# Performance work log

Measured on AMD Instinct MI355X. Metric: run time of the kernel, lower is better.

The kernel has to match this reference:

```python
import jax, jax.numpy as jnp
import numpy as np

IN_FEATURES = 1024
OUT_FEATURES = 1024
NUM_GRIDS = 8
GRID_MIN, GRID_MAX = -2.0, 2.0
DENOM = (GRID_MAX - GRID_MIN) / (NUM_GRIDS - 1)
LN_EPS = 1e-5
GRID = jnp.linspace(GRID_MIN, GRID_MAX, NUM_GRIDS)


def setup_inputs() -> dict:
    key = jax.random.key(0)
    k_x, k_sw, k_bw = jax.random.split(key, 3)
    N = 8192
    x = jax.random.normal(k_x, (N, IN_FEATURES), dtype=jnp.float32)
    ln_gamma = jnp.ones((IN_FEATURES,), dtype=jnp.float32)
    ln_beta = jnp.zeros((IN_FEATURES,), dtype=jnp.float32)
    # trunc_normal(std=0.1) approximated by scaled normal
    spline_w = 0.1 * jax.random.normal(k_sw, (OUT_FEATURES, IN_FEATURES * NUM_GRIDS), dtype=jnp.float32)
    base_w = jax.random.normal(k_bw, (OUT_FEATURES, IN_FEATURES), dtype=jnp.float32) * (1.0 / np.sqrt(IN_FEATURES))
    base_b = jnp.zeros((OUT_FEATURES,), dtype=jnp.float32)
    return {"x": x, "ln_gamma": ln_gamma, "ln_beta": ln_beta,
            "spline_w": spline_w, "base_w": base_w, "base_b": base_b}


def reference(x, ln_gamma, ln_beta, spline_w, base_w, base_b):
    # LayerNorm over last dim
    mu = jnp.mean(x, axis=-1, keepdims=True)
    var = jnp.var(x, axis=-1, keepdims=True)
    xn = (x - mu) * jax.lax.rsqrt(var + LN_EPS) * ln_gamma + ln_beta
    # RBF basis: [N, in, G]
    basis = jnp.exp(-jnp.square((xn[..., None] - GRID) / DENOM))
    basis = basis.reshape(x.shape[0], IN_FEATURES * NUM_GRIDS)
    y = jnp.einsum('nk,ok->no', basis, spline_w)
    y = y + jnp.einsum('nd,od->no', jax.nn.silu(x), base_w) + base_b
    return y
```

## Files before the change

kernel.cpp:

```cpp
#include <hip/hip_runtime.h>
#include <hip/hip_bf16.h>
#include <stdint.h>

#define IN_F 1024
#define OUT_F 1024
#define NG 8
#define KSPLINE 8192
#define KDIM 9216
#define KHALF 4608
#define M_ROWS 8192
#define LOG2E 1.4426950408889634f
#define KC 2.1019642153762872f

#define A_BLOCKS (M_ROWS / 4)
#define W_BLOCKS ((OUT_F * 2304) / 256)
#define RB (KDIM * 2)

using half4v = __attribute__((ext_vector_type(4))) _Float16;
using half8  = __attribute__((ext_vector_type(8))) _Float16;
using f32x4  = __attribute__((ext_vector_type(4))) float;

#define AS1 __attribute__((address_space(1)))
#define AS3 __attribute__((address_space(3)))

__global__ __launch_bounds__(256) void prep_kernel(
        const float* __restrict__ x, const float* __restrict__ gamma,
        const float* __restrict__ beta, const float* __restrict__ sw,
        const float* __restrict__ bw, _Float16* __restrict__ A,
        _Float16* __restrict__ W) {
    if (blockIdx.x >= A_BLOCKS) {
        int idx = (blockIdx.x - A_BLOCKS) * 256 + threadIdx.x;
        int o   = idx / 2304;
        int k4  = idx - o * 2304;
        float4 v;
        if (k4 < 2048) v = ((const float4*)sw)[(size_t)o * 2048 + k4];
        else           v = ((const float4*)bw)[(size_t)o * 256 + (k4 - 2048)];
        half4v h = { (_Float16)v.x, (_Float16)v.y, (_Float16)v.z, (_Float16)v.w };
        *(half4v*)(W + (size_t)idx * 4) = h;
        return;
    }
    const int wave = threadIdx.x >> 6, lane = threadIdx.x & 63;
    const int row = blockIdx.x * 4 + wave;
    const float* xr = x + (size_t)row * IN_F;

    float xv[16];
    float s = 0.0f, s2 = 0.0f;
#pragma unroll
    for (int j = 0; j < 16; ++j) {
        float v = xr[j * 64 + lane];
        xv[j] = v;
        s += v;
        s2 += v * v;
    }
#pragma unroll
    for (int off = 32; off > 0; off >>= 1) {
        s  += __shfl_xor(s, off);
        s2 += __shfl_xor(s2, off);
    }
    float mu   = s * (1.0f / IN_F);
    float var  = s2 * (1.0f / IN_F) - mu * mu;
    float rstd = rsqrtf(var + 1e-5f);

    const float cq[8] = {
        -2.0000000f * KC, -1.4285715f * KC, -0.8571429f * KC, -0.2857143f * KC,
         0.2857143f * KC,  0.8571429f * KC,  1.4285715f * KC,  2.0000000f * KC };

    _Float16* Arow = A + (size_t)row * KDIM;
    half8* basis_out = (half8*)Arow;
    _Float16* silu_out = Arow + KSPLINE;
#pragma unroll
    for (int j = 0; j < 16; ++j) {
        int f = j * 64 + lane;
        float xs = xv[j];
        float xq = ((xs - mu) * rstd * gamma[f] + beta[f]) * KC;
        half8 h;
#pragma unroll
        for (int g = 0; g < 8; ++g) {
            float v = xq - cq[g];
            h[g] = (_Float16)exp2f(-(v * v));
        }
        basis_out[f] = h;
        silu_out[f] = (_Float16)(xs / (1.0f + exp2f(-xs * LOG2E)));
    }
}

__global__ __launch_bounds__(512, 2) void gemm_kernel(
        const _Float16* __restrict__ A, const _Float16* __restrict__ W,
        const float* __restrict__ bias, float* __restrict__ C,
        float* __restrict__ P, int ntiles, int gpz) {
    extern __shared__ __align__(16) char smem[];
    const int tid  = threadIdx.x;
    const int wave = tid >> 6, lane = tid & 63;
    const int wm = wave >> 2, wn = wave & 3;

    const int lb = blockIdx.x;
    const int per_xcd = gridDim.x >> 5;
    const int xcd = lb & 7, sl = lb >> 3;
    const int g  = xcd * per_xcd + (sl >> 2);
    const int bn = sl & 3;
    const int bm = g / gpz;
    const int z  = g - bm * gpz;

    const int l8 = lane >> 3;
    const int srcswz = ((lane & 7) ^ l8) << 4;
    const char* pA = (const char*)A + (size_t)(bm * 256 + wave * 8 + l8) * RB
                     + (size_t)z * (KHALF * 2) + srcswz;
    const char* pB = (const char*)W + (size_t)(bn * 256 + wave * 8 + l8) * RB
                     + (size_t)z * (KHALF * 2) + srcswz;
    const int dstOff = wave * 1024;

    const int lm  = lane & 15;
    const int hi  = (lane >> 4) << 4;
    const int swz = (lm & 7) << 4;
    const int aoff0 = (wm * 128 + lm) * 128 + ((0  + hi) ^ swz);
    const int aoff1 = (wm * 128 + lm) * 128 + ((64 + hi) ^ swz);
    const int boff0 = 32768 + (wn * 64 + lm) * 128 + ((0  + hi) ^ swz);
    const int boff1 = 32768 + (wn * 64 + lm) * 128 + ((64 + hi) ^ swz);

    f32x4 acc[8][4] = {};

#pragma unroll
    for (int j = 0; j < 4; ++j) {
        __builtin_amdgcn_global_load_lds((const AS1 void*)(pA + (size_t)j * 64 * RB),
            (AS3 void*)(smem + j * 8192 + dstOff), 16, 0, 0);
        __builtin_amdgcn_global_load_lds((const AS1 void*)(pB + (size_t)j * 64 * RB),
            (AS3 void*)(smem + 32768 + j * 8192 + dstOff), 16, 0, 0);
    }

    for (int kt = 0; kt < ntiles; ++kt) {
        char* sbuf = smem + (kt & 1) * 65536;
        char* nbuf = smem + ((kt & 1) ^ 1) * 65536;

        if (kt + 1 < ntiles) {
            const size_t kb = (size_t)(kt + 1) * 128;
#pragma unroll
            for (int j = 0; j < 4; ++j) {
                __builtin_amdgcn_global_load_lds((const AS1 void*)(pA + (size_t)j * 64 * RB + kb),
                    (AS3 void*)(nbuf + j * 8192 + dstOff), 16, 0, 0);
                __builtin_amdgcn_global_load_lds((const AS1 void*)(pB + (size_t)j * 64 * RB + kb),
                    (AS3 void*)(nbuf + 32768 + j * 8192 + dstOff), 16, 0, 0);
            }
            asm volatile("s_waitcnt vmcnt(8)" ::: "memory");
        } else {
            asm volatile("s_waitcnt vmcnt(0)" ::: "memory");
        }
        __builtin_amdgcn_s_barrier();

        half8 b[4][2];
#pragma unroll
        for (int nf = 0; nf < 4; ++nf) {
            b[nf][0] = *(const half8*)(sbuf + boff0 + nf * 2048);
            b[nf][1] = *(const half8*)(sbuf + boff1 + nf * 2048);
        }
        {
            half8 a00 = *(const half8*)(sbuf + aoff0);
            half8 a01 = *(const half8*)(sbuf + aoff1);
            half8 a10 = *(const half8*)(sbuf + aoff0 + 2048);
            half8 a11 = *(const half8*)(sbuf + aoff1 + 2048);
            __builtin_amdgcn_s_barrier();
            asm volatile("s_waitcnt lgkmcnt(0)" ::: "memory");
            __builtin_amdgcn_sched_barrier(0);
            __builtin_amdgcn_s_setprio(1);
#pragma unroll
            for (int nf = 0; nf < 4; ++nf) {
                acc[0][nf] = __builtin_amdgcn_mfma_f32_16x16x32_f16(a00, b[nf][0], acc[0][nf], 0, 0, 0);
                acc[1][nf] = __builtin_amdgcn_mfma_f32_16x16x32_f16(a10, b[nf][0], acc[1][nf], 0, 0, 0);
            }
#pragma unroll
            for (int nf = 0; nf < 4; ++nf) {
                acc[0][nf] = __builtin_amdgcn_mfma_f32_16x16x32_f16(a01, b[nf][1], acc[0][nf], 0, 0, 0);
                acc[1][nf] = __builtin_amdgcn_mfma_f32_16x16x32_f16(a11, b[nf][1], acc[1][nf], 0, 0, 0);
            }
            __builtin_amdgcn_s_setprio(0);
            __builtin_amdgcn_s_barrier();
        }
#pragma unroll
        for (int p = 1; p < 4; ++p) {
            half8 a00 = *(const half8*)(sbuf + aoff0 + (2 * p) * 2048);
            half8 a01 = *(const half8*)(sbuf + aoff1 + (2 * p) * 2048);
            half8 a10 = *(const half8*)(sbuf + aoff0 + (2 * p + 1) * 2048);
            half8 a11 = *(const half8*)(sbuf + aoff1 + (2 * p + 1) * 2048);
            __builtin_amdgcn_s_barrier();
            asm volatile("s_waitcnt lgkmcnt(0)" ::: "memory");
            __builtin_amdgcn_sched_barrier(0);
            __builtin_amdgcn_s_setprio(1);
#pragma unroll
            for (int nf = 0; nf < 4; ++nf) {
                acc[2*p][nf]   = __builtin_amdgcn_mfma_f32_16x16x32_f16(a00, b[nf][0], acc[2*p][nf], 0, 0, 0);
                acc[2*p+1][nf] = __builtin_amdgcn_mfma_f32_16x16x32_f16(a10, b[nf][0], acc[2*p+1][nf], 0, 0, 0);
            }
#pragma unroll
            for (int nf = 0; nf < 4; ++nf) {
                acc[2*p][nf]   = __builtin_amdgcn_mfma_f32_16x16x32_f16(a01, b[nf][1], acc[2*p][nf], 0, 0, 0);
                acc[2*p+1][nf] = __builtin_amdgcn_mfma_f32_16x16x32_f16(a11, b[nf][1], acc[2*p+1][nf], 0, 0, 0);
            }
            __builtin_amdgcn_s_setprio(0);
            __builtin_amdgcn_s_barrier();
        }
    }

    const int cn  = lane & 15;
    const int rm4 = (lane >> 4) * 4;
    float* dst = z ? P : C;
#pragma unroll
    for (int nf = 0; nf < 4; ++nf) {
        int col = bn * 256 + wn * 64 + nf * 16 + cn;
        float bv = z ? 0.0f : bias[col];
#pragma unroll
        for (int mf = 0; mf < 8; ++mf) {
            int row = bm * 256 + wm * 128 + mf * 16 + rm4;
            float* cp = dst + (size_t)row * OUT_F + col;
#pragma unroll
            for (int r = 0; r < 4; ++r)
                cp[(size_t)r * OUT_F] = acc[mf][nf][r] + bv;
        }
    }
}

__global__ __launch_bounds__(256) void reduce_kernel(float* __restrict__ C,
        const float* __restrict__ P) {
    const int n4 = M_ROWS * OUT_F / 4;
    float4* c4 = (float4*)C;
    const float4* p4 = (const float4*)P;
    for (int i = blockIdx.x * 256 + threadIdx.x; i < n4; i += 2048 * 256) {
        float4 a = c4[i];
        float4 b = p4[i];
        a.x += b.x; a.y += b.y; a.z += b.z; a.w += b.w;
        c4[i] = a;
    }
}

extern "C" void kernel_launch(void* const* d_in, const int* in_sizes, int n_in,
                              void* d_out, int out_size, void* d_ws, size_t ws_size,
                              hipStream_t stream) {
    const float* x     = (const float*)d_in[0];
    const float* gamma = (const float*)d_in[1];
    const float* beta  = (const float*)d_in[2];
    const float* sw    = (const float*)d_in[3];
    const float* bw    = (const float*)d_in[4];
    const float* bb    = (const float*)d_in[5];
    float* out = (float*)d_out;

    char* ws = (char*)d_ws;
    size_t offW = 0;
    size_t offA = (size_t)OUT_F * KDIM * 2;
    size_t offP = offA + (size_t)M_ROWS * KDIM * 2;
    size_t need = offP + (size_t)M_ROWS * OUT_F * 4;
    _Float16* Wb = (_Float16*)(ws + offW);
    _Float16* Ab = (_Float16*)(ws + offA);
    float*    Pb = (float*)(ws + offP);
    const int split = (ws_size >= need);

    static int s_attr = 0;
    if (!s_attr) {
        hipFuncSetAttribute(reinterpret_cast<const void*>(gemm_kernel),
                            hipFuncAttributeMaxDynamicSharedMemorySize, 131072);
        s_attr = 1;
    }

    prep_kernel<<<A_BLOCKS + W_BLOCKS, 256, 0, stream>>>(
        x, gamma, beta, sw, bw, Ab, Wb);
    if (split) {
        gemm_kernel<<<256, 512, 131072, stream>>>(Ab, Wb, bb, out, Pb, KHALF / 64, 2);
        reduce_kernel<<<2048, 256, 0, stream>>>(out, Pb);
    } else {
        gemm_kernel<<<128, 512, 131072, stream>>>(Ab, Wb, bb, out, Pb, KDIM / 64, 1);
    }
}
```

Before: 297.1 us.

## Split GEMM K-tile into quadrant phases with staggered per-stage prefetch

Reorganizes the main MFMA loop of the GEMM into four quadrant phases (A-half × B-half). Each phase computes on fragments already in registers, and the next tile's global→LDS loads are issued in per-stage pairs interleaved between the phases. The LDS row mapping of A and B stages is permuted so that each quadrant's operands come from specific stages, which allows finer-grained vmcnt waits instead of one wait for the whole next tile. The aim is better overlap of memory traffic with MFMA work and fewer stalls. In exchange there are more barriers per iteration and tighter waitcnt bookkeeping.

```diff
diff --git a/kernel.cpp b/kernel.cpp
--- a/kernel.cpp
+++ b/kernel.cpp
@@ -102,101 +102,151 @@
     const int z  = g - bm * gpz;
 
     const int l8 = lane >> 3;
-    const int srcswz = ((lane & 7) ^ l8) << 4;
-    const char* pA = (const char*)A + (size_t)(bm * 256 + wave * 8 + l8) * RB
-                     + (size_t)z * (KHALF * 2) + srcswz;
-    const char* pB = (const char*)W + (size_t)(bn * 256 + wave * 8 + l8) * RB
-                     + (size_t)z * (KHALF * 2) + srcswz;
-    const int dstOff = wave * 1024;
+    const int chunkswz = ((lane & 7) ^ l8) << 4;
+    const size_t zoff = (size_t)z * (KHALF * 2);
+    const int gA[4] = {0, 128, 64, 192};
+    const int gB[4] = {0, 128, 32, 160};
+    const char* pA[4];
+    const char* pB[4];
+#pragma unroll
+    for (int s = 0; s < 4; ++s) {
+        pA[s] = (const char*)A + (size_t)(bm * 256 + gA[s] + wave * 8 + l8) * RB
+                + zoff + chunkswz;
+        pB[s] = (const char*)W + (size_t)(bn * 256 + gB[s] + (wave >> 2) * 64
+                + (wave & 3) * 8 + l8) * RB + zoff + chunkswz;
+    }
+
+#define STAGE_A(s, nb, colb) __builtin_amdgcn_global_load_lds( \
+        (const AS1 void*)(pA[s] + (colb)), \
+        (AS3 void*)(smem + (nb) + (s) * 8192 + wave * 1024), 16, 0, 0)
+#define STAGE_B(s, nb, colb) __builtin_amdgcn_global_load_lds( \
+        (const AS1 void*)(pB[s] + (colb)), \
+        (AS3 void*)(smem + (nb) + 32768 + (s) * 8192 + wave * 1024), 16, 0, 0)
 
     const int lm  = lane & 15;
     const int hi  = (lane >> 4) << 4;
     const int swz = (lm & 7) << 4;
-    const int aoff0 = (wm * 128 + lm) * 128 + ((0  + hi) ^ swz);
-    const int aoff1 = (wm * 128 + lm) * 128 + ((64 + hi) ^ swz);
-    const int boff0 = 32768 + (wn * 64 + lm) * 128 + ((0  + hi) ^ swz);
-    const int boff1 = 32768 + (wn * 64 + lm) * 128 + ((64 + hi) ^ swz);
+    const int ck0 = (0  + hi) ^ swz;
+    const int ck1 = (64 + hi) ^ swz;
+    const int aB0 = (0 + wm) * 8192 + lm * 128;
+    const int aB1 = (2 + wm) * 8192 + lm * 128;
+    const int bB0 = 32768 + (0 + (wn >> 1)) * 8192 + ((wn & 1) * 32 + lm) * 128;
+    const int bB1 = 32768 + (2 + (wn >> 1)) * 8192 + ((wn & 1) * 32 + lm) * 128;
 
     f32x4 acc[8][4] = {};
 
-#pragma unroll
-    for (int j = 0; j < 4; ++j) {
-        __builtin_amdgcn_global_load_lds((const AS1 void*)(pA + (size_t)j * 64 * RB),
-            (AS3 void*)(smem + j * 8192 + dstOff), 16, 0, 0);
-        __builtin_amdgcn_global_load_lds((const AS1 void*)(pB + (size_t)j * 64 * RB),
-            (AS3 void*)(smem + 32768 + j * 8192 + dstOff), 16, 0, 0);
-    }
+    STAGE_A(0, 0, 0); STAGE_A(1, 0, 0);
+    STAGE_B(0, 0, 0); STAGE_B(1, 0, 0);
+    STAGE_B(2, 0, 0); STAGE_B(3, 0, 0);
+    STAGE_A(2, 0, 0); STAGE_A(3, 0, 0);
+    asm volatile("s_waitcnt vmcnt(4)" ::: "memory");
+    __builtin_amdgcn_s_barrier();
 
     for (int kt = 0; kt < ntiles; ++kt) {
-        char* sbuf = smem + (kt & 1) * 65536;
-        char* nbuf = smem + ((kt & 1) ^ 1) * 65536;
-
-        if (kt + 1 < ntiles) {
-            const size_t kb = (size_t)(kt + 1) * 128;
-#pragma unroll
-            for (int j = 0; j < 4; ++j) {
-                __builtin_amdgcn_global_load_lds((const AS1 void*)(pA + (size_t)j * 64 * RB + kb),
-                    (AS3 void*)(nbuf + j * 8192 + dstOff), 16, 0, 0);
-                __builtin_amdgcn_global_load_lds((const AS1 void*)(pB + (size_t)j * 64 * RB + kb),
-                    (AS3 void*)(nbuf + 32768 + j * 8192 + dstOff), 16, 0, 0);
-            }
-            asm volatile("s_waitcnt vmcnt(8)" ::: "memory");
+        const int cb = (kt & 1) * 65536;
+        const int nb = cb ^ 65536;
+        const size_t col = (size_t)(kt + 1) * 128;
+        const bool pref = (kt + 1 < ntiles);
+
+        half8 aF[4][2], bF[2][2];
+#pragma unroll
+        for (int m = 0; m < 4; ++m) {
+            aF[m][0] = *(const half8*)(smem + cb + aB0 + m * 2048 + ck0);
+            aF[m][1] = *(const half8*)(smem + cb + aB0 + m * 2048 + ck1);
+        }
+#pragma unroll
+        for (int n = 0; n < 2; ++n) {
+            bF[n][0] = *(const half8*)(smem + cb + bB0 + n * 2048 + ck0);
+            bF[n][1] = *(const half8*)(smem + cb + bB0 + n * 2048 + ck1);
+        }
+        asm volatile("s_waitcnt vmcnt(2)" ::: "memory");
+        if (pref) { STAGE_A(0, nb, col); STAGE_A(1, nb, col); }
+        asm volatile("s_waitcnt lgkmcnt(8)" ::: "memory");
+        __builtin_amdgcn_s_barrier();
+        asm volatile("s_waitcnt lgkmcnt(0)" ::: "memory");
+        __builtin_amdgcn_s_setprio(1);
+#pragma unroll
+        for (int n = 0; n < 2; ++n)
+#pragma unroll
+            for (int m = 0; m < 4; ++m)
+                acc[m][n] = __builtin_amdgcn_mfma_f32_16x16x32_f16(aF[m][0], bF[n][0], acc[m][n], 0, 0, 0);
+#pragma unroll
+        for (int n = 0; n < 2; ++n)
+#pragma unroll
+            for (int m = 0; m < 4; ++m)
+                acc[m][n] = __builtin_amdgcn_mfma_f32_16x16x32_f16(aF[m][1], bF[n][1], acc[m][n], 0, 0, 0);
+        __builtin_amdgcn_s_setprio(0);
+        __builtin_amdgcn_s_barrier();
+
+        half8 bG[2][2];
+#pragma unroll
+        for (int n = 0; n < 2; ++n) {
+            bG[n][0] = *(const half8*)(smem + cb + bB1 + n * 2048 + ck0);
+            bG[n][1] = *(const half8*)(smem + cb + bB1 + n * 2048 + ck1);
+        }
+        if (pref) {
+            asm volatile("s_waitcnt vmcnt(2)" ::: "memory");
+            STAGE_B(0, nb, col); STAGE_B(1, nb, col);
         } else {
             asm volatile("s_waitcnt vmcnt(0)" ::: "memory");
         }
         __builtin_amdgcn_s_barrier();
-
-        half8 b[4][2];
-#pragma unroll
-        for (int nf = 0; nf < 4; ++nf) {
-            b[nf][0] = *(const half8*)(sbuf + boff0 + nf * 2048);
-            b[nf][1] = *(const half8*)(sbuf + boff1 + nf * 2048);
-        }
-        {
-            half8 a00 = *(const half8*)(sbuf + aoff0);
-            half8 a01 = *(const half8*)(sbuf + aoff1);
-            half8 a10 = *(const half8*)(sbuf + aoff0 + 2048);
-            half8 a11 = *(const half8*)(sbuf + aoff1 + 2048);
-            __builtin_amdgcn_s_barrier();
-            asm volatile("s_waitcnt lgkmcnt(0)" ::: "memory");
-            __builtin_amdgcn_sched_barrier(0);
-            __builtin_amdgcn_s_setprio(1);
-#pragma unroll
-            for (int nf = 0; nf < 4; ++nf) {
-                acc[0][nf] = __builtin_amdgcn_mfma_f32_16x16x32_f16(a00, b[nf][0], acc[0][nf], 0, 0, 0);
-                acc[1][nf] = __builtin_amdgcn_mfma_f32_16x16x32_f16(a10, b[nf][0], acc[1][nf], 0, 0, 0);
-            }
-#pragma unroll
-            for (int nf = 0; nf < 4; ++nf) {
-                acc[0][nf] = __builtin_amdgcn_mfma_f32_16x16x32_f16(a01, b[nf][1], acc[0][nf], 0, 0, 0);
-                acc[1][nf] = __builtin_amdgcn_mfma_f32_16x16x32_f16(a11, b[nf][1], acc[1][nf], 0, 0, 0);
-            }
-            __builtin_amdgcn_s_setprio(0);
-            __builtin_amdgcn_s_barrier();
-        }
-#pragma unroll
-        for (int p = 1; p < 4; ++p) {
-            half8 a00 = *(const half8*)(sbuf + aoff0 + (2 * p) * 2048);
-            half8 a01 = *(const half8*)(sbuf + aoff1 + (2 * p) * 2048);
-            half8 a10 = *(const half8*)(sbuf + aoff0 + (2 * p + 1) * 2048);
-            half8 a11 = *(const half8*)(sbuf + aoff1 + (2 * p + 1) * 2048);
-            __builtin_amdgcn_s_barrier();
-            asm volatile("s_waitcnt lgkmcnt(0)" ::: "memory");
-            __builtin_amdgcn_sched_barrier(0);
-            __builtin_amdgcn_s_setprio(1);
-#pragma unroll
-            for (int nf = 0; nf < 4; ++nf) {
-                acc[2*p][nf]   = __builtin_amdgcn_mfma_f32_16x16x32_f16(a00, b[nf][0], acc[2*p][nf], 0, 0, 0);
-                acc[2*p+1][nf] = __builtin_amdgcn_mfma_f32_16x16x32_f16(a10, b[nf][0], acc[2*p+1][nf], 0, 0, 0);
-            }
-#pragma unroll
-            for (int nf = 0; nf < 4; ++nf) {
-                acc[2*p][nf]   = __builtin_amdgcn_mfma_f32_16x16x32_f16(a01, b[nf][1], acc[2*p][nf], 0, 0, 0);
-                acc[2*p+1][nf] = __builtin_amdgcn_mfma_f32_16x16x32_f16(a11, b[nf][1], acc[2*p+1][nf], 0, 0, 0);
-            }
-            __builtin_amdgcn_s_setprio(0);
-            __builtin_amdgcn_s_barrier();
-        }
+        asm volatile("s_waitcnt lgkmcnt(0)" ::: "memory");
+        __builtin_amdgcn_s_setprio(1);
+#pragma unroll
+        for (int n = 0; n < 2; ++n)
+#pragma unroll
+            for (int m = 0; m < 4; ++m)
+                acc[m][2 + n] = __builtin_amdgcn_mfma_f32_16x16x32_f16(aF[m][0], bG[n][0], acc[m][2 + n], 0, 0, 0);
+#pragma unroll
+        for (int n = 0; n < 2; ++n)
+#pragma unroll
+            for (int m = 0; m < 4; ++m)
+                acc[m][2 + n] = __builtin_amdgcn_mfma_f32_16x16x32_f16(aF[m][1], bG[n][1], acc[m][2 + n], 0, 0, 0);
+        __builtin_amdgcn_s_setprio(0);
+        __builtin_amdgcn_s_barrier();
+
+        half8 aG[4][2];
+#pragma unroll
+        for (int m = 0; m < 4; ++m) {
+            aG[m][0] = *(const half8*)(smem + cb + aB1 + m * 2048 + ck0);
+            aG[m][1] = *(const half8*)(smem + cb + aB1 + m * 2048 + ck1);
+        }
+        if (pref) { STAGE_B(2, nb, col); STAGE_B(3, nb, col); }
+        __builtin_amdgcn_s_barrier();
+        asm volatile("s_waitcnt lgkmcnt(0)" ::: "memory");
+        __builtin_amdgcn_s_setprio(1);
+#pragma unroll
+        for (int n = 0; n < 2; ++n)
+#pragma unroll
+            for (int m = 0; m < 4; ++m)
+                acc[4 + m][n] = __builtin_amdgcn_mfma_f32_16x16x32_f16(aG[m][0], bF[n][0], acc[4 + m][n], 0, 0, 0);
+#pragma unroll
+        for (int n = 0; n < 2; ++n)
+#pragma unroll
+            for (int m = 0; m < 4; ++m)
+                acc[4 + m][n] = __builtin_amdgcn_mfma_f32_16x16x32_f16(aG[m][1], bF[n][1], acc[4 + m][n], 0, 0, 0);
+        __builtin_amdgcn_s_setprio(0);
+        __builtin_amdgcn_s_barrier();
+
+        if (pref) {
+            asm volatile("s_waitcnt vmcnt(2)" ::: "memory");
+            STAGE_A(2, nb, col); STAGE_A(3, nb, col);
+        }
+        __builtin_amdgcn_s_barrier();
+        __builtin_amdgcn_s_setprio(1);
+#pragma unroll
+        for (int n = 0; n < 2; ++n)
+#pragma unroll
+            for (int m = 0; m < 4; ++m)
+                acc[4 + m][2 + n] = __builtin_amdgcn_mfma_f32_16x16x32_f16(aG[m][0], bG[n][0], acc[4 + m][2 + n], 0, 0, 0);
+#pragma unroll
+        for (int n = 0; n < 2; ++n)
+#pragma unroll
+            for (int m = 0; m < 4; ++m)
+                acc[4 + m][2 + n] = __builtin_amdgcn_mfma_f32_16x16x32_f16(aG[m][1], bG[n][1], acc[4 + m][2 + n], 0, 0, 0);
+        __builtin_amdgcn_s_setprio(0);
+        __builtin_amdgcn_s_barrier();
     }
 
     const int cn  = lane & 15;
```

After: 287.8 us. -3.1%, faster.
